# Kernel optimization log

Hardware: AMD Instinct MI355X
Metric: run time of the kernel (lower is better)

The kernel has to match this reference:

```python
import jax, jax.numpy as jnp
import numpy as np

N_NODES = 100000
N_EDGES = 500000
HIDDEN = 32
HEADS = 4
PROJ = HIDDEN * HEADS  # 128
LN_EPS = 1e-5


def setup_inputs() -> dict:
    key = jax.random.key(0)
    ks = jax.random.split(key, 12)
    # Xavier-uniform bound for Linear(3, PROJ): sqrt(6/(3+PROJ))
    b_qkv = float(np.sqrt(6.0 / (3 + PROJ)))
    b_out = float(np.sqrt(6.0 / (PROJ + HIDDEN)))
    return {
        "positions": jax.random.normal(ks[0], (N_NODES, 3), dtype=jnp.float32),
        "edge_index": jax.random.randint(ks[1], (2, N_EDGES), 0, N_NODES, dtype=jnp.int64),
        "Wq": jax.random.uniform(ks[2], (3, PROJ), jnp.float32, -b_qkv, b_qkv),
        "bq": jnp.zeros((PROJ,), jnp.float32),
        "Wk": jax.random.uniform(ks[3], (3, PROJ), jnp.float32, -b_qkv, b_qkv),
        "bk": jnp.zeros((PROJ,), jnp.float32),
        "Wv": jax.random.uniform(ks[4], (3, PROJ), jnp.float32, -b_qkv, b_qkv),
        "bv": jnp.zeros((PROJ,), jnp.float32),
        "Wout": jax.random.uniform(ks[5], (PROJ, HIDDEN), jnp.float32, -b_out, b_out),
        "bout": jnp.zeros((HIDDEN,), jnp.float32),
        "gamma": jnp.ones((HIDDEN,), jnp.float32),
        "beta": jnp.zeros((HIDDEN,), jnp.float32),
    }


def reference(positions, edge_index, Wq, bq, Wk, bk, Wv, bv, Wout, bout, gamma, beta):
    row, col = edge_index[0], edge_index[1]
    rel = positions[row] - positions[col]                      # [E, 3]
    E = rel.shape[0]
    q = (rel @ Wq + bq).reshape(E, HEADS, HIDDEN)              # [E, H, D]
    k = (rel @ Wk + bk).reshape(E, HEADS, HIDDEN)
    v = (rel @ Wv + bv).reshape(E, HEADS, HIDDEN)
    # attention score per (edge, head), softmax over heads
    scores = jnp.sum(q * k, axis=-1) / jnp.sqrt(jnp.float32(HIDDEN))  # [E, H]
    attn = jax.nn.softmax(scores, axis=-1)                     # dropout is identity in eval
    wv = (attn[..., None] * v).reshape(E, PROJ)                # [E, H*D]
    # scatter-mean over destination nodes (col), dim_size = N
    seg_sum = jax.ops.segment_sum(wv, col, num_segments=N_NODES)
    counts = jax.ops.segment_sum(jnp.ones((E,), wv.dtype), col, num_segments=N_NODES)
    mean = seg_sum / jnp.maximum(counts, 1.0)[:, None]         # [N, H*D]
    out = mean @ Wout + bout                                   # [N, D]
    mu = jnp.mean(out, axis=-1, keepdims=True)
    var = jnp.var(out, axis=-1, keepdims=True)
    out = (out - mu) / jnp.sqrt(var + LN_EPS) * gamma + beta
    return jax.nn.silu(out)
```

## Files before the change

kernel.cpp:

```cpp
#include <hip/hip_runtime.h>
#include <hip/hip_bf16.h>

#define LN_EPS 1e-5f


__global__ void precompute_kernel(const float* __restrict__ Wq,
                                  const float* __restrict__ bq,
                                  const float* __restrict__ Wk,
                                  const float* __restrict__ bk,
                                  const float* __restrict__ Wv,
                                  const float* __restrict__ bv,
                                  const float* __restrict__ Wout,
                                  const int* __restrict__ ei,
                                  float* __restrict__ flag,
                                  float* __restrict__ coef,
                                  float* __restrict__ T) {
  __shared__ float sM[4][3][32];
  __shared__ float sCv[4][32];
  int t = threadIdx.x;
  const float scale = 0.17677669529663687f;

  if (t == 0) {
    int all_zero = 1;
    for (int i = 0; i < 8; ++i) all_zero &= (ei[2 * i + 1] == 0);
    flag[0] = all_zero ? 1.0f : 0.0f;
  }

  {
    int h = t >> 5, o = t & 31;
    float m0 = 0, m1 = 0, m2 = 0, cv = 0;
    for (int d = 0; d < 32; ++d) {
      int j = h * 32 + d;
      float w = Wout[j * 32 + o];
      m0 += Wv[0 * 128 + j] * w;
      m1 += Wv[1 * 128 + j] * w;
      m2 += Wv[2 * 128 + j] * w;
      cv += bv[j] * w;
    }
    sM[h][0][o] = m0;
    sM[h][1][o] = m1;
    sM[h][2][o] = m2;
    sCv[h][o] = cv;
  }

  if (t < 40) {
    int h = t / 10, j = t % 10;
    float acc = 0;
    for (int d = 0; d < 32; ++d) {
      int idx = h * 32 + d;
      float q0 = Wq[0 * 128 + idx], q1 = Wq[1 * 128 + idx], q2 = Wq[2 * 128 + idx];
      float k0 = Wk[0 * 128 + idx], k1 = Wk[1 * 128 + idx], k2 = Wk[2 * 128 + idx];
      float bqv = bq[idx], bkv = bk[idx];
      float v;
      switch (j) {
        case 0: v = q0 * k0; break;
        case 1: v = q1 * k1; break;
        case 2: v = q2 * k2; break;
        case 3: v = q0 * k1 + q1 * k0; break;
        case 4: v = q0 * k2 + q2 * k0; break;
        case 5: v = q1 * k2 + q2 * k1; break;
        case 6: v = q0 * bkv + k0 * bqv; break;
        case 7: v = q1 * bkv + k1 * bqv; break;
        case 8: v = q2 * bkv + k2 * bqv; break;
        default: v = bqv * bkv; break;
      }
      acc += v;
    }
    coef[h * 10 + j] = acc * scale;
  }

  __syncthreads();

  for (int idx = t; idx < 512; idx += 128) {
    int j = idx >> 5, col = idx & 31;
    float v;
    if (j < 3)        v = sCv[j][col] - sCv[3][col];
    else if (j < 6)   v = sM[3][j - 3][col];
    else if (j < 15)  { int h = (j - 6) / 3, i = (j - 6) % 3; v = sM[h][i][col] - sM[3][i][col]; }
    else              v = sCv[3][col];
    T[idx] = v;
  }
}

__global__ void edge_kernel(const float* __restrict__ pos,
                            const int* __restrict__ ei, int E,
                            const float* __restrict__ flag,
                            const float* __restrict__ coef,
                            float* __restrict__ fsums) {
  const int lane = threadIdx.x & 31;
  const int group = (blockIdx.x * blockDim.x + threadIdx.x) >> 5;
  const int base = group * 32;
  if (base >= E) return;

  const int i64 = (flag[0] != 0.0f) ? 1 : 0;
  const int valid_n = min(32, E - base);
  const int e = base + lane;

  int c = 0;
  float rx = 0, ry = 0, rz = 0, a0 = 0, a1 = 0, a2 = 0;
  if (lane < valid_n) {
    int r, cc;
    if (i64) {
      r = ei[2 * (size_t)e];
      cc = ei[2 * ((size_t)E + e)];
    } else {
      r = ei[e];
      cc = ei[E + e];
    }
    c = cc;
    rx = pos[r * 3 + 0] - pos[cc * 3 + 0];
    ry = pos[r * 3 + 1] - pos[cc * 3 + 1];
    rz = pos[r * 3 + 2] - pos[cc * 3 + 2];
    float s[4];
#pragma unroll
    for (int h = 0; h < 4; ++h) {
      const float* cf = coef + h * 10;
      s[h] = cf[9] + rx * cf[6] + ry * cf[7] + rz * cf[8] + rx * rx * cf[0] +
             ry * ry * cf[1] + rz * rz * cf[2] + rx * ry * cf[3] +
             rx * rz * cf[4] + ry * rz * cf[5];
    }
    float mx = fmaxf(fmaxf(s[0], s[1]), fmaxf(s[2], s[3]));
    float e0 = __expf(s[0] - mx), e1 = __expf(s[1] - mx);
    float e2 = __expf(s[2] - mx), e3 = __expf(s[3] - mx);
    float inv = 1.0f / (e0 + e1 + e2 + e3);
    a0 = e0 * inv; a1 = e1 * inv; a2 = e2 * inv;
  }

  const int comp = lane & 15;
  int pa, pr;
  if (comp < 3)       { pa = comp;          pr = 3; }
  else if (comp < 6)  { pa = 3;             pr = comp - 3; }
  else if (comp < 15) { pa = (comp - 6) / 3; pr = (comp - 6) % 3; }
  else                { pa = 3;             pr = 3; }
  const int sub = lane >> 4;

  for (int t2 = 0; t2 < valid_n; t2 += 2) {
    const int src = t2 + sub;
    float tx = __shfl(rx, src, 32);
    float ty = __shfl(ry, src, 32);
    float tz = __shfl(rz, src, 32);
    float b0 = __shfl(a0, src, 32);
    float b1 = __shfl(a1, src, 32);
    float b2 = __shfl(a2, src, 32);
    int   ct = __shfl(c,  src, 32);
    float A = (pa == 0) ? b0 : (pa == 1) ? b1 : (pa == 2) ? b2 : 1.0f;
    float R = (pr == 0) ? tx : (pr == 1) ? ty : (pr == 2) ? tz : 1.0f;
    if (src < valid_n)
      atomicAdd(&fsums[(size_t)ct * 16 + comp], A * R);
  }
}

__global__ void node_kernel(const float* __restrict__ fsums,
                            const float* __restrict__ T,
                            const float* __restrict__ bout,
                            const float* __restrict__ gamma,
                            const float* __restrict__ beta,
                            float* __restrict__ out, int N) {
  int tid = blockIdx.x * blockDim.x + threadIdx.x;
  int node = tid >> 5;
  int col = tid & 31;
  if (node >= N) return;

  float myf = fsums[(size_t)node * 16 + (col & 15)];
  float cnt = __shfl(myf, 15, 32);
  float invc = 1.0f / fmaxf(cnt, 1.0f);

  float acc = bout[col];
#pragma unroll
  for (int j = 0; j < 16; ++j) {
    float fj = __shfl(myf, j, 32);
    acc = fmaf(fj * invc, T[j * 32 + col], acc);
  }

  float sx = acc, sx2 = acc * acc;
#pragma unroll
  for (int off = 16; off >= 1; off >>= 1) {
    sx += __shfl_xor(sx, off);
    sx2 += __shfl_xor(sx2, off);
  }
  float mu = sx * (1.0f / 32.0f);
  float var = sx2 * (1.0f / 32.0f) - mu * mu;
  float inv = rsqrtf(var + LN_EPS);
  float y = (acc - mu) * inv * gamma[col] + beta[col];
  float o = y * (1.0f / (1.0f + __expf(-y)));
  out[(size_t)node * 32 + col] = o;
}

extern "C" void kernel_launch(void* const* d_in, const int* in_sizes, int n_in,
                              void* d_out, int out_size, void* d_ws, size_t ws_size,
                              hipStream_t stream) {
  const float* pos  = (const float*)d_in[0];
  const int*   ei   = (const int*)d_in[1];
  const float* Wq   = (const float*)d_in[2];
  const float* bq   = (const float*)d_in[3];
  const float* Wk   = (const float*)d_in[4];
  const float* bk   = (const float*)d_in[5];
  const float* Wv   = (const float*)d_in[6];
  const float* bv   = (const float*)d_in[7];
  const float* Wout = (const float*)d_in[8];
  const float* bout = (const float*)d_in[9];
  const float* gam  = (const float*)d_in[10];
  const float* bet  = (const float*)d_in[11];

  const int N = in_sizes[0] / 3;
  const int E = in_sizes[1] / 2;

  float* ws    = (float*)d_ws;
  float* fsums = ws;
  float* flag  = fsums + (size_t)N * 16;
  float* coef  = flag + 8;
  float* T     = coef + 40;

  hipMemsetAsync(d_ws, 0, (size_t)N * 16 * sizeof(float), stream);

  precompute_kernel<<<1, 128, 0, stream>>>(Wq, bq, Wk, bk, Wv, bv, Wout, ei,
                                           flag, coef, T);

  int edge_blocks = (E + 255) / 256;
  edge_kernel<<<edge_blocks, 256, 0, stream>>>(pos, ei, E, flag, coef, fsums);

  int node_blocks = (int)(((size_t)N * 32 + 255) / 256);
  node_kernel<<<node_blocks, 256, 0, stream>>>(fsums, T, bout, gam, bet,
                                               (float*)d_out, N);

  (void)n_in; (void)out_size; (void)ws_size;
}
```

Measured before the change: 145.6 us.

## Bucket-sort edges by destination and reduce with shared-memory atomics

Replaces per-edge global float atomics with a counting sort. Edges are split into buckets of 512 destination nodes using per-block histograms, a scan and a permute through shared memory. Each reduce block then accumulates its bucket's features with LDS atomics and fuses the node projection, layernorm and SiLU, which removes the workspace memset and the separate node pass. Per-edge payloads (rel vector and attention weights) are packed to fp16 to halve scratch traffic. This trades accuracy for bandwidth and adds three launches. It assumes no bucket exceeds the fixed capacity of 4096 edges.

```diff
diff --git a/kernel.cpp b/kernel.cpp
--- a/kernel.cpp
+++ b/kernel.cpp
@@ -1,7 +1,29 @@
 #include <hip/hip_runtime.h>
 #include <hip/hip_bf16.h>
+#include <hip/hip_fp16.h>
 
 #define LN_EPS 1e-5f
+#define NBK   256
+#define SHIFT 9
+#define BW    512
+#define CAP   4096
+#define CHMAX 1024
+
+__device__ __forceinline__ unsigned pk2(float a, float b) {
+  _Float16 ha = (_Float16)a, hb = (_Float16)b;
+  unsigned short ua = *(unsigned short*)&ha, ub = *(unsigned short*)&hb;
+  return (unsigned)ua | ((unsigned)ub << 16);
+}
+__device__ __forceinline__ float lo16(unsigned u) {
+  unsigned short s = (unsigned short)(u & 0xffff);
+  _Float16 h = *(_Float16*)&s;
+  return (float)h;
+}
+__device__ __forceinline__ float hi16(unsigned u) {
+  unsigned short s = (unsigned short)(u >> 16);
+  _Float16 h = *(_Float16*)&s;
+  return (float)h;
+}
 
 
 __global__ void precompute_kernel(const float* __restrict__ Wq,
@@ -82,108 +104,226 @@
   }
 }
 
-__global__ void edge_kernel(const float* __restrict__ pos,
-                            const int* __restrict__ ei, int E,
-                            const float* __restrict__ flag,
-                            const float* __restrict__ coef,
-                            float* __restrict__ fsums) {
-  const int lane = threadIdx.x & 31;
-  const int group = (blockIdx.x * blockDim.x + threadIdx.x) >> 5;
-  const int base = group * 32;
-  if (base >= E) return;
+__global__ void edge_compute_kernel(const float* __restrict__ pos,
+                                    const int* __restrict__ ei, int E, int chunk,
+                                    const float* __restrict__ flag,
+                                    const float* __restrict__ coef,
+                                    uint4* __restrict__ scratch,
+                                    int* __restrict__ hist) {
+  __shared__ int lhist[NBK];
+  const int tid = threadIdx.x;
+  for (int i = tid; i < NBK; i += 256) lhist[i] = 0;
+  __syncthreads();
 
   const int i64 = (flag[0] != 0.0f) ? 1 : 0;
-  const int valid_n = min(32, E - base);
-  const int e = base + lane;
-
-  int c = 0;
-  float rx = 0, ry = 0, rz = 0, a0 = 0, a1 = 0, a2 = 0;
-  if (lane < valid_n) {
-    int r, cc;
+  const int start = blockIdx.x * chunk;
+  const int end = min(start + chunk, E);
+
+  float cf[40];
+#pragma unroll
+  for (int i = 0; i < 40; ++i) cf[i] = coef[i];
+
+  for (int e = start + tid; e < end; e += 256) {
+    int r, c;
     if (i64) {
       r = ei[2 * (size_t)e];
-      cc = ei[2 * ((size_t)E + e)];
+      c = ei[2 * ((size_t)E + e)];
     } else {
       r = ei[e];
-      cc = ei[E + e];
-    }
-    c = cc;
-    rx = pos[r * 3 + 0] - pos[cc * 3 + 0];
-    ry = pos[r * 3 + 1] - pos[cc * 3 + 1];
-    rz = pos[r * 3 + 2] - pos[cc * 3 + 2];
+      c = ei[E + e];
+    }
+    float rx = pos[r * 3 + 0] - pos[c * 3 + 0];
+    float ry = pos[r * 3 + 1] - pos[c * 3 + 1];
+    float rz = pos[r * 3 + 2] - pos[c * 3 + 2];
     float s[4];
 #pragma unroll
     for (int h = 0; h < 4; ++h) {
-      const float* cf = coef + h * 10;
-      s[h] = cf[9] + rx * cf[6] + ry * cf[7] + rz * cf[8] + rx * rx * cf[0] +
-             ry * ry * cf[1] + rz * rz * cf[2] + rx * ry * cf[3] +
-             rx * rz * cf[4] + ry * rz * cf[5];
+      const float* f = cf + h * 10;
+      s[h] = f[9] + rx * f[6] + ry * f[7] + rz * f[8] + rx * rx * f[0] +
+             ry * ry * f[1] + rz * rz * f[2] + rx * ry * f[3] +
+             rx * rz * f[4] + ry * rz * f[5];
     }
     float mx = fmaxf(fmaxf(s[0], s[1]), fmaxf(s[2], s[3]));
     float e0 = __expf(s[0] - mx), e1 = __expf(s[1] - mx);
     float e2 = __expf(s[2] - mx), e3 = __expf(s[3] - mx);
     float inv = 1.0f / (e0 + e1 + e2 + e3);
-    a0 = e0 * inv; a1 = e1 * inv; a2 = e2 * inv;
-  }
+    float a0 = e0 * inv, a1 = e1 * inv, a2 = e2 * inv;
+
+    atomicAdd(&lhist[c >> SHIFT], 1);
+    uint4 w;
+    w.x = (unsigned)c;
+    w.y = pk2(rx, ry);
+    w.z = pk2(rz, a0);
+    w.w = pk2(a1, a2);
+    scratch[e] = w;
+  }
+  __syncthreads();
+  for (int i = tid; i < NBK; i += 256) hist[blockIdx.x * NBK + i] = lhist[i];
+}
+
+__global__ void scan_kernel(const int* __restrict__ hist,
+                            int* __restrict__ offs,
+                            int* __restrict__ count, int nb1) {
+  const int k = blockIdx.x;
+  const int lane = threadIdx.x;
+  int carry = 0;
+  for (int j0 = 0; j0 < nb1; j0 += 64) {
+    int j = j0 + lane;
+    int v = (j < nb1) ? hist[(size_t)j * NBK + k] : 0;
+    int s = v;
+#pragma unroll
+    for (int off = 1; off < 64; off <<= 1) {
+      int t = __shfl_up(s, off);
+      if (lane >= off) s += t;
+    }
+    if (j < nb1) offs[(size_t)j * NBK + k] = k * CAP + carry + (s - v);
+    carry += __shfl(s, 63);
+  }
+  if (lane == 0) count[k] = carry;
+}
+
+__global__ void permute_kernel(const uint4* __restrict__ scratch,
+                               const int* __restrict__ offs,
+                               int E, int chunk,
+                               uint4* __restrict__ queue) {
+  __shared__ uint4 stage[CHMAX];
+  __shared__ int lcnt[NBK];
+  __shared__ int lstart[NBK];
+  __shared__ int goff[NBK];
+  const int tid = threadIdx.x;
+
+  for (int i = tid; i < NBK; i += 256) {
+    lcnt[i] = 0;
+    goff[i] = offs[(size_t)blockIdx.x * NBK + i];
+  }
+  __syncthreads();
+
+  const int start = blockIdx.x * chunk;
+  const int end = min(start + chunk, E);
+  const int n = end - start;
+
+  uint4 pw[4];
+  int slot[4];
+  int nee = 0;
+  for (int e = start + tid; e < end; e += 256) {
+    uint4 w = scratch[e];
+    pw[nee] = w;
+    slot[nee] = atomicAdd(&lcnt[w.x >> SHIFT], 1);
+    ++nee;
+  }
+  __syncthreads();
+
+  if (tid < 64) {
+    int carry = 0;
+    for (int b0 = 0; b0 < NBK; b0 += 64) {
+      int v = lcnt[b0 + tid];
+      int s = v;
+#pragma unroll
+      for (int off = 1; off < 64; off <<= 1) {
+        int t = __shfl_up(s, off);
+        if (tid >= off) s += t;
+      }
+      lstart[b0 + tid] = carry + (s - v);
+      carry += __shfl(s, 63);
+    }
+  }
+  __syncthreads();
+
+  for (int i = 0; i < nee; ++i)
+    stage[lstart[pw[i].x >> SHIFT] + slot[i]] = pw[i];
+  __syncthreads();
+
+  for (int i = tid; i < n; i += 256) {
+    uint4 w = stage[i];
+    int b = w.x >> SHIFT;
+    queue[goff[b] + (i - lstart[b])] = w;
+  }
+}
+
+__device__ __forceinline__ void sel_comp(int comp, int& pa, int& pr) {
+  if (comp < 3)       { pa = comp;           pr = 3; }
+  else if (comp < 6)  { pa = 3;              pr = comp - 3; }
+  else if (comp < 15) { pa = (comp - 6) / 3; pr = (comp - 6) % 3; }
+  else                { pa = 3;              pr = 3; }
+}
+
+__global__ void reduce_kernel(const uint4* __restrict__ queue,
+                              const int* __restrict__ count,
+                              const float* __restrict__ T,
+                              const float* __restrict__ bout,
+                              const float* __restrict__ gamma,
+                              const float* __restrict__ beta,
+                              float* __restrict__ out, int N) {
+  __shared__ float acc[BW * 16];
+  const int k = blockIdx.x;
+  const int tid = threadIdx.x;
+  const int lane = tid & 31;
+  const int grp = tid >> 5;
+
+  for (int i = tid; i < BW * 16; i += 256) acc[i] = 0.0f;
+
+  const int col = tid & 31;
+  float Tcol[16];
+#pragma unroll
+  for (int j = 0; j < 16; ++j) Tcol[j] = T[j * 32 + col];
+  const float bo = bout[col], ga = gamma[col], be = beta[col];
+
+  __syncthreads();
+
+  const int cnt = count[k];
+  const uint4* q = queue + (size_t)k * CAP;
 
   const int comp = lane & 15;
+  const int sub = lane >> 4;
   int pa, pr;
-  if (comp < 3)       { pa = comp;          pr = 3; }
-  else if (comp < 6)  { pa = 3;             pr = comp - 3; }
-  else if (comp < 15) { pa = (comp - 6) / 3; pr = (comp - 6) % 3; }
-  else                { pa = 3;             pr = 3; }
-  const int sub = lane >> 4;
-
-  for (int t2 = 0; t2 < valid_n; t2 += 2) {
-    const int src = t2 + sub;
-    float tx = __shfl(rx, src, 32);
-    float ty = __shfl(ry, src, 32);
-    float tz = __shfl(rz, src, 32);
-    float b0 = __shfl(a0, src, 32);
-    float b1 = __shfl(a1, src, 32);
-    float b2 = __shfl(a2, src, 32);
-    int   ct = __shfl(c,  src, 32);
-    float A = (pa == 0) ? b0 : (pa == 1) ? b1 : (pa == 2) ? b2 : 1.0f;
-    float R = (pr == 0) ? tx : (pr == 1) ? ty : (pr == 2) ? tz : 1.0f;
-    if (src < valid_n)
-      atomicAdd(&fsums[(size_t)ct * 16 + comp], A * R);
-  }
-}
-
-__global__ void node_kernel(const float* __restrict__ fsums,
-                            const float* __restrict__ T,
-                            const float* __restrict__ bout,
-                            const float* __restrict__ gamma,
-                            const float* __restrict__ beta,
-                            float* __restrict__ out, int N) {
-  int tid = blockIdx.x * blockDim.x + threadIdx.x;
-  int node = tid >> 5;
-  int col = tid & 31;
-  if (node >= N) return;
-
-  float myf = fsums[(size_t)node * 16 + (col & 15)];
-  float cnt = __shfl(myf, 15, 32);
-  float invc = 1.0f / fmaxf(cnt, 1.0f);
-
-  float acc = bout[col];
-#pragma unroll
-  for (int j = 0; j < 16; ++j) {
-    float fj = __shfl(myf, j, 32);
-    acc = fmaf(fj * invc, T[j * 32 + col], acc);
-  }
-
-  float sx = acc, sx2 = acc * acc;
-#pragma unroll
-  for (int off = 16; off >= 1; off >>= 1) {
-    sx += __shfl_xor(sx, off);
-    sx2 += __shfl_xor(sx2, off);
-  }
-  float mu = sx * (1.0f / 32.0f);
-  float var = sx2 * (1.0f / 32.0f) - mu * mu;
-  float inv = rsqrtf(var + LN_EPS);
-  float y = (acc - mu) * inv * gamma[col] + beta[col];
-  float o = y * (1.0f / (1.0f + __expf(-y)));
-  out[(size_t)node * 32 + col] = o;
+  sel_comp(comp, pa, pr);
+
+  for (int gbase = grp * 32; gbase < cnt; gbase += 256) {
+    const int valid_n = min(32, cnt - gbase);
+    uint4 w = (lane < valid_n) ? q[gbase + lane] : uint4{0, 0, 0, 0};
+    for (int t2 = 0; t2 < valid_n; t2 += 2) {
+      const int src = t2 + sub;
+      int wx = __shfl((int)w.x, src, 32);
+      int wy = __shfl((int)w.y, src, 32);
+      int wz = __shfl((int)w.z, src, 32);
+      int ww = __shfl((int)w.w, src, 32);
+      float tx = lo16(wy), ty = hi16(wy);
+      float tz = lo16(wz), b0 = hi16(wz);
+      float b1 = lo16(ww), b2 = hi16(ww);
+      float A = (pa == 0) ? b0 : (pa == 1) ? b1 : (pa == 2) ? b2 : 1.0f;
+      float R = (pr == 0) ? tx : (pr == 1) ? ty : (pr == 2) ? tz : 1.0f;
+      if (src < valid_n)
+        atomicAdd(&acc[((unsigned)wx & (BW - 1)) * 16 + comp], A * R);
+    }
+  }
+  __syncthreads();
+
+  const int node0 = k * BW;
+  const int nodes_here = min(BW, N - node0);
+  for (int idx = tid; idx < nodes_here * 32; idx += 256) {
+    int node_l = idx >> 5;
+    float myf = acc[node_l * 16 + (col & 15)];
+    float cntn = __shfl(myf, 15, 32);
+    float invc = 1.0f / fmaxf(cntn, 1.0f);
+    float a = bo;
+#pragma unroll
+    for (int j = 0; j < 16; ++j) {
+      float fj = __shfl(myf, j, 32);
+      a = fmaf(fj * invc, Tcol[j], a);
+    }
+    float sx = a, sx2 = a * a;
+#pragma unroll
+    for (int off = 16; off >= 1; off >>= 1) {
+      sx += __shfl_xor(sx, off);
+      sx2 += __shfl_xor(sx2, off);
+    }
+    float mu = sx * (1.0f / 32.0f);
+    float var = sx2 * (1.0f / 32.0f) - mu * mu;
+    float inv = rsqrtf(var + LN_EPS);
+    float y = (a - mu) * inv * ga + be;
+    float o = y * (1.0f / (1.0f + __expf(-y)));
+    out[(size_t)(node0 + node_l) * 32 + col] = o;
+  }
 }
 
 extern "C" void kernel_launch(void* const* d_in, const int* in_sizes, int n_in,
@@ -205,23 +345,28 @@
   const int N = in_sizes[0] / 3;
   const int E = in_sizes[1] / 2;
 
-  float* ws    = (float*)d_ws;
-  float* fsums = ws;
-  float* flag  = fsums + (size_t)N * 16;
-  float* coef  = flag + 8;
-  float* T     = coef + 40;
-
-  hipMemsetAsync(d_ws, 0, (size_t)N * 16 * sizeof(float), stream);
+  const int nb1 = (E + CHMAX - 1) / CHMAX;
+  const int chunk = (E + nb1 - 1) / nb1;
+  const int nbuk = (N + BW - 1) / BW;
+
+  char* p = (char*)d_ws;
+  uint4* scratch = (uint4*)p;                        p += (size_t)E * 16;
+  uint4* queue   = (uint4*)p;                        p += (size_t)NBK * CAP * 16;
+  int*   hist    = (int*)p;                          p += (size_t)1024 * NBK * 4;
+  int*   offs    = (int*)p;                          p += (size_t)1024 * NBK * 4;
+  int*   cnt     = (int*)p;                          p += 4096;
+  float* flag    = (float*)p;
+  float* coef    = flag + 8;
+  float* T       = coef + 40;
 
   precompute_kernel<<<1, 128, 0, stream>>>(Wq, bq, Wk, bk, Wv, bv, Wout, ei,
                                            flag, coef, T);
-
-  int edge_blocks = (E + 255) / 256;
-  edge_kernel<<<edge_blocks, 256, 0, stream>>>(pos, ei, E, flag, coef, fsums);
-
-  int node_blocks = (int)(((size_t)N * 32 + 255) / 256);
-  node_kernel<<<node_blocks, 256, 0, stream>>>(fsums, T, bout, gam, bet,
-                                               (float*)d_out, N);
+  edge_compute_kernel<<<nb1, 256, 0, stream>>>(pos, ei, E, chunk, flag, coef,
+                                               scratch, hist);
+  scan_kernel<<<NBK, 64, 0, stream>>>(hist, offs, cnt, nb1);
+  permute_kernel<<<nb1, 256, 0, stream>>>(scratch, offs, E, chunk, queue);
+  reduce_kernel<<<nbuk, 256, 0, stream>>>(queue, cnt, T, bout, gam, bet,
+                                          (float*)d_out, N);
 
   (void)n_in; (void)out_size; (void)ws_size;
 }
```

After: 245.6 us. +68.7%, slower.
